# Kernel optimization log

Hardware: AMD Instinct MI355X
Metric: run time of the kernel (lower is better)

## Reference

```python
import jax, jax.numpy as jnp
import numpy as np

B, D, N, K, H = 32, 1024, 65536, 4096, 8

def setup_inputs() -> dict:
    key = jax.random.key(0)
    ks = jax.random.split(key, 8)
    s = D ** -0.5  # keep projections well-scaled
    return {
        "query": jax.random.normal(ks[0], (B, D), jnp.float32),
        "buffer": jax.random.normal(ks[1], (N, D), jnp.float32),
        "priorities": jax.random.normal(ks[2], (N,), jnp.float32),
        "Wq": jax.random.normal(ks[3], (D, D), jnp.float32) * s,
        "bq": jnp.zeros((D,), jnp.float32),
        "Wk": jax.random.normal(ks[4], (D, D), jnp.float32) * s,
        "bk": jnp.zeros((D,), jnp.float32),
        "Wv": jax.random.normal(ks[5], (D, D), jnp.float32) * s,
        "bv": jnp.zeros((D,), jnp.float32),
        "Wo": jax.random.normal(ks[6], (D, D), jnp.float32) * s,
        "bo": jnp.zeros((D,), jnp.float32),
        "top_k": K,
    }

def reference(query, buffer, priorities, Wq, bq, Wk, bk, Wv, bv, Wo, bo, top_k):
    # priority-based top-k selection (no_grad in original)
    _, idx = jax.lax.top_k(jax.lax.stop_gradient(priorities), top_k)
    subset = buffer[idx]                              # [K, D] gather; shared across batch
    hd = D // H
    scale = hd ** -0.5
    q = (query @ Wq + bq).reshape(B, H, hd)           # single-query attention (seq len 1)
    k = (subset @ Wk + bk).reshape(top_k, H, hd)
    v = (subset @ Wv + bv).reshape(top_k, H, hd)
    scores = jnp.einsum('bhd,khd->bhk', q, k) * scale  # [B, H, K]
    attn = jax.nn.softmax(scores, axis=-1)
    ctx = jnp.einsum('bhk,khd->bhd', attn, v).reshape(B, D)
    retrieved = ctx @ Wo + bo                          # [B, D]
    attn_avg = attn.mean(axis=1)                       # head-averaged weights [B, K]
    return retrieved, attn_avg
```

## Files before the change

kernel.cpp:

```cpp
#include <hip/hip_runtime.h>
#include <stdint.h>

typedef unsigned int u32;
typedef unsigned long long u64;
typedef uint16_t u16;

typedef short bf16x8 __attribute__((ext_vector_type(8)));
typedef float f32x4 __attribute__((ext_vector_type(4)));


__device__ __forceinline__ float bf2f(u16 x) { return __uint_as_float(((u32)x) << 16); }
__device__ __forceinline__ u16 f2bf(float f) {
    u32 u = __float_as_uint(f);
    return (u16)((u + 0x7FFF + ((u >> 16) & 1)) >> 16);
}


__global__ __launch_bounds__(256) void init_kernel(const float* __restrict__ prio,
                                                   u64* __restrict__ keys,
                                                   u32* __restrict__ hist,
                                                   u64* __restrict__ cand,
                                                   u32* __restrict__ scctl) {
    int i = blockIdx.x * 256 + threadIdx.x;
    u32 fb = __float_as_uint(prio[i]);
    u32 s = (fb & 0x80000000u) ? ~fb : (fb | 0x80000000u);
    keys[i] = ((u64)(~s) << 32) | (u64)i;
    hist[i] = 0;
    if (i < 8192) cand[i] = ~0ull;
    if (i < 4) scctl[i] = 0;
}

__global__ __launch_bounds__(256) void hist_kernel(const u64* __restrict__ keys,
                                                   u32* __restrict__ hist) {
    int i = blockIdx.x * 256 + threadIdx.x;
    atomicAdd(&hist[(u32)(keys[i] >> 48)], 1u);
}

__global__ __launch_bounds__(1024) void scan_kernel(const u32* __restrict__ hist,
                                                    u32* __restrict__ scctl) {
    int t = threadIdx.x;
    int base = t * 64;
    const uint4* hp = (const uint4*)(hist + base);
    u32 s = 0;
#pragma unroll
    for (int i = 0; i < 16; ++i) {
        uint4 h4 = hp[i];
        s += h4.x + h4.y + h4.z + h4.w;
    }
    u32 inc = s;
    for (int o = 1; o < 64; o <<= 1) {
        u32 v = __shfl_up(inc, o);
        if ((t & 63) >= o) inc += v;
    }
    __shared__ u32 ws[16];
    if ((t & 63) == 63) ws[t >> 6] = inc;
    __syncthreads();
    if (t == 0) {
        u32 a = 0;
        for (int wv = 0; wv < 16; ++wv) { u32 x = ws[wv]; ws[wv] = a; a += x; }
    }
    __syncthreads();
    u32 incl = inc + ws[t >> 6];
    u32 excl = incl - s;
    if (excl < 4096u && incl >= 4096u) {
        u32 cum = excl;
        for (int i = 0; i < 64; ++i) {
            u32 c = hist[base + i];
            if (cum + c >= 4096u) { scctl[0] = (u32)(base + i); scctl[1] = cum; break; }
            cum += c;
        }
    }
}

__global__ __launch_bounds__(256) void compact_kernel(const u64* __restrict__ keys,
                                                      u64* __restrict__ cand,
                                                      u32* __restrict__ scctl) {
    int i = blockIdx.x * 256 + threadIdx.x;
    u64 k = keys[i];
    u32 bin = (u32)(k >> 48);
    u32 Tb = scctl[0];
    if (bin < Tb) {
        u32 p = atomicAdd(&scctl[2], 1u);
        cand[p] = k;
    } else if (bin == Tb) {
        u32 p = atomicAdd(&scctl[3], 1u);
        if (p < 4096u) cand[4096 + p] = k;
    }
}

__global__ __launch_bounds__(1024) void sort4096_kernel(u64* __restrict__ cand) {
    __shared__ u64 sh[4096];
    u64* src = cand + (size_t)blockIdx.x * 4096;
    int t = threadIdx.x;
    u64 v[4];
#pragma unroll
    for (int s = 0; s < 4; ++s) v[s] = src[t * 4 + s];
    for (int k = 2; k <= 4096; k <<= 1) {
        for (int j = k >> 1; j >= 1; j >>= 1) {
            if (j >= 256) {
                __syncthreads();
#pragma unroll
                for (int s = 0; s < 4; ++s) sh[t * 4 + s] = v[s];
                __syncthreads();
#pragma unroll
                for (int s = 0; s < 4; ++s) {
                    int i = t * 4 + s;
                    u64 p = sh[i ^ j];
                    bool keepmin = (((i & k) == 0) == ((i & j) == 0));
                    v[s] = keepmin ? (v[s] < p ? v[s] : p) : (v[s] > p ? v[s] : p);
                }
            } else if (j >= 4) {
                int ld = j >> 2;
#pragma unroll
                for (int s = 0; s < 4; ++s) {
                    int i = t * 4 + s;
                    u64 p = __shfl_xor(v[s], ld, 64);
                    bool keepmin = (((i & k) == 0) == ((i & j) == 0));
                    v[s] = keepmin ? (v[s] < p ? v[s] : p) : (v[s] > p ? v[s] : p);
                }
            } else if (j == 2) {
#pragma unroll
                for (int s = 0; s < 2; ++s) {
                    int i = t * 4 + s;
                    bool up = ((i & k) == 0);
                    u64 a = v[s], b = v[s + 2];
                    if ((a > b) == up) { v[s] = b; v[s + 2] = a; }
                }
            } else {
#pragma unroll
                for (int s = 0; s < 4; s += 2) {
                    int i = t * 4 + s;
                    bool up = ((i & k) == 0);
                    u64 a = v[s], b = v[s + 1];
                    if ((a > b) == up) { v[s] = b; v[s + 1] = a; }
                }
            }
        }
    }
#pragma unroll
    for (int s = 0; s < 4; ++s) src[t * 4 + s] = v[s];
}

__global__ __launch_bounds__(256) void gather_transpose_kernel(const float* __restrict__ buffer,
                                                               const u64* __restrict__ cand,
                                                               const u32* __restrict__ scctl,
                                                               u16* __restrict__ bsub,
                                                               u16* __restrict__ bsubT) {
    int r0 = blockIdx.x * 32;
    int t = threadIdx.x;
    __shared__ u16 tile[32][65];
    __shared__ u32 rowidx[32];
    if (t < 32) {
        int row = r0 + t;
        u32 S = scctl[1];
        u64 key = ((u32)row < S) ? cand[row] : cand[4096 + row - (int)S];
        rowidx[t] = (u32)key;
    }
    __syncthreads();
    for (int c0 = 0; c0 < 1024; c0 += 64) {
        for (int s = t; s < 512; s += 256) {
            int r = s >> 4, c4 = (s & 15) * 4;
            float4 vv = *(const float4*)(buffer + (size_t)rowidx[r] * 1024 + c0 + c4);
            ushort4 o;
            o.x = f2bf(vv.x); o.y = f2bf(vv.y); o.z = f2bf(vv.z); o.w = f2bf(vv.w);
            *(ushort4*)(bsub + (size_t)(r0 + r) * 1024 + c0 + c4) = o;
            tile[r][c4] = o.x; tile[r][c4 + 1] = o.y; tile[r][c4 + 2] = o.z; tile[r][c4 + 3] = o.w;
        }
        __syncthreads();
        for (int s = t; s < 1024; s += 256) {
            int rT = s >> 4;
            int cT = (s & 15) * 2;
            ushort2 o2;
            o2.x = tile[cT][rT];
            o2.y = tile[cT + 1][rT];
            *(ushort2*)(bsubT + (size_t)(c0 + rT) * 4096 + r0 + cT) = o2;
        }
        __syncthreads();
    }
}

__global__ __launch_bounds__(256) void vecmat4_kernel(const float* __restrict__ X,
                                                      const float* __restrict__ W,
                                                      const float* __restrict__ bias,
                                                      float* __restrict__ out) {
    int bg = blockIdx.x, n0 = blockIdx.y * 64, t = threadIdx.x;
    __shared__ float xs[4][1024];
    __shared__ float red[4][4][64];
    for (int s = t; s < 4096; s += 256) {
        int bb = s >> 10, k = s & 1023;
        xs[bb][k] = X[(bg * 4 + bb) * 1024 + k];
    }
    __syncthreads();
    int n = t & 63, kq = t >> 6;
    const float* Wp = W + (size_t)(kq * 256) * 1024 + n0 + n;
    const float* x0 = xs[0] + kq * 256;
    const float* x1 = xs[1] + kq * 256;
    const float* x2 = xs[2] + kq * 256;
    const float* x3 = xs[3] + kq * 256;
    float a0 = 0.f, a1 = 0.f, a2 = 0.f, a3 = 0.f;
#pragma unroll 8
    for (int k = 0; k < 256; ++k) {
        float w = Wp[(size_t)k * 1024];
        a0 += x0[k] * w; a1 += x1[k] * w; a2 += x2[k] * w; a3 += x3[k] * w;
    }
    red[kq][0][n] = a0; red[kq][1][n] = a1; red[kq][2][n] = a2; red[kq][3][n] = a3;
    __syncthreads();
    int bb = t >> 6;
    out[(bg * 4 + bb) * 1024 + n0 + n] =
        red[0][bb][n] + red[1][bb][n] + red[2][bb][n] + red[3][bb][n] + bias[n0 + n];
}

__global__ __launch_bounds__(256) void s1_kernel(const float* __restrict__ qp,
                                                 const float* __restrict__ Wk,
                                                 const float* __restrict__ bk,
                                                 u16* __restrict__ S1,
                                                 float* __restrict__ cb) {
    int h = blockIdx.x, e0 = blockIdx.y * 64, t = threadIdx.x;
    __shared__ float qsh[32][128];
    __shared__ float wsh[64][132];
    for (int s = t; s < 4096; s += 256) {
        int b = s >> 7, d = s & 127;
        qsh[b][d] = qp[b * 1024 + h * 128 + d];
    }
    for (int s = t; s < 8192; s += 256) {
        int e = s >> 7, d = s & 127;
        wsh[e][d] = Wk[(size_t)(e0 + e) * 1024 + h * 128 + d];
    }
    __syncthreads();
    if (blockIdx.y == 0 && t < 32) {
        float a = 0.f;
        for (int d = 0; d < 128; ++d) a += qsh[t][d] * bk[h * 128 + d];
        cb[t * 8 + h] = a;
    }
    int e = t & 63, b0 = (t >> 6) * 8;
    float acc[8] = {0.f, 0.f, 0.f, 0.f, 0.f, 0.f, 0.f, 0.f};
#pragma unroll 4
    for (int d = 0; d < 128; d += 4) {
        float4 w = *(const float4*)&wsh[e][d];
#pragma unroll
        for (int bb = 0; bb < 8; ++bb) {
            float4 q = *(const float4*)&qsh[b0 + bb][d];
            acc[bb] += w.x * q.x + w.y * q.y + w.z * q.z + w.w * q.w;
        }
    }
#pragma unroll
    for (int bb = 0; bb < 8; ++bb)
        S1[(size_t)((b0 + bb) * 8 + h) * 1024 + e0 + e] = f2bf(acc[bb]);
}

__global__ __launch_bounds__(256) void gemm_scores_kernel(const u16* __restrict__ A,
                                                          const u16* __restrict__ B,
                                                          const float* __restrict__ cb,
                                                          float* __restrict__ out) {
    const int nt = blockIdx.x, mt = blockIdx.y;
    __shared__ __align__(16) u16 As[128 * 64];
    __shared__ __align__(16) u16 Bs[128 * 64];
    const int t = threadIdx.x, lane = t & 63, w = t >> 6;
    const int wm = (w >> 1) * 64, wn = (w & 1) * 64;
    const int q16 = lane >> 4, l15 = lane & 15;
    f32x4 acc[4][4];
#pragma unroll
    for (int i = 0; i < 4; i++)
#pragma unroll
        for (int j = 0; j < 4; j++) acc[i][j] = (f32x4){0.f, 0.f, 0.f, 0.f};
    const int sr = t >> 3, sc = t & 7;
    for (int kk = 0; kk < 1024; kk += 64) {
#pragma unroll
        for (int p = 0; p < 4; ++p) {
            int r = p * 32 + sr, pc = sc ^ (r & 7);
            uint4 va = *(const uint4*)(A + (size_t)(mt * 128 + r) * 1024 + kk + sc * 8);
            uint4 vb = *(const uint4*)(B + (size_t)(nt * 128 + r) * 1024 + kk + sc * 8);
            *(uint4*)&As[r * 64 + pc * 8] = va;
            *(uint4*)&Bs[r * 64 + pc * 8] = vb;
        }
        __syncthreads();
#pragma unroll
        for (int f = 0; f < 2; ++f) {
            bf16x8 a[4], b[4];
#pragma unroll
            for (int i = 0; i < 4; ++i) {
                int m = wm + i * 16 + l15;
                int pc = (f * 4 + q16) ^ (m & 7);
                a[i] = *(const bf16x8*)&As[m * 64 + pc * 8];
                int n = wn + i * 16 + l15;
                b[i] = *(const bf16x8*)&Bs[n * 64 + pc * 8];
            }
#pragma unroll
            for (int i = 0; i < 4; ++i)
#pragma unroll
                for (int j = 0; j < 4; ++j)
                    acc[i][j] = __builtin_amdgcn_mfma_f32_16x16x32_bf16(a[i], b[j], acc[i][j], 0, 0, 0);
        }
        __syncthreads();
    }
#pragma unroll
    for (int i = 0; i < 4; ++i) {
        int mbase = mt * 128 + wm + i * 16 + q16 * 4;
        float cbv[4];
#pragma unroll
        for (int r = 0; r < 4; ++r) cbv[r] = cb[mbase + r];
#pragma unroll
        for (int j = 0; j < 4; ++j) {
            int n = nt * 128 + wn + j * 16 + l15;
#pragma unroll
            for (int r = 0; r < 4; ++r)
                out[(size_t)(mbase + r) * 4096 + n] = acc[i][j][r] * 0.08838834764831845f + cbv[r];
        }
    }
}

__global__ __launch_bounds__(256) void softmax_kernel(const float* __restrict__ scores,
                                                      u16* __restrict__ attnbf) {
    int row = blockIdx.x, t = threadIdx.x;
    __shared__ float rowsh[4096];
    __shared__ float red[4];
    const float* p = scores + (size_t)row * 4096;
    float m = -1e30f;
    for (int i = t; i < 4096; i += 256) {
        float v = p[i];
        rowsh[i] = v;
        m = fmaxf(m, v);
    }
#pragma unroll
    for (int o = 32; o >= 1; o >>= 1) m = fmaxf(m, __shfl_xor(m, o));
    if ((t & 63) == 0) red[t >> 6] = m;
    __syncthreads();
    m = fmaxf(fmaxf(red[0], red[1]), fmaxf(red[2], red[3]));
    float sum = 0.f;
    for (int i = t; i < 4096; i += 256) {
        float e = __expf(rowsh[i] - m);
        rowsh[i] = e;
        sum += e;
    }
#pragma unroll
    for (int o = 32; o >= 1; o >>= 1) sum += __shfl_xor(sum, o);
    __syncthreads();
    if ((t & 63) == 0) red[t >> 6] = sum;
    __syncthreads();
    sum = red[0] + red[1] + red[2] + red[3];
    float inv = 1.0f / sum;
    for (int i = t; i < 4096; i += 256)
        attnbf[(size_t)row * 4096 + i] = f2bf(rowsh[i] * inv);
}

__global__ void attn_avg_kernel(const u16* __restrict__ attnbf,
                                float* __restrict__ out) {
    int g = blockIdx.x * 256 + threadIdx.x;
    int b = g >> 12, k = g & 4095;
    float s = 0.f;
#pragma unroll
    for (int h = 0; h < 8; ++h) s += bf2f(attnbf[(size_t)(b * 8 + h) * 4096 + k]);
    out[g] = s * 0.125f;
}

__global__ __launch_bounds__(256) void gemm_t_kernel(const u16* __restrict__ A,
                                                     const u16* __restrict__ B,
                                                     float* __restrict__ part) {
    const int nt = blockIdx.x, mt = blockIdx.y, ks = blockIdx.z;
    __shared__ __align__(16) u16 As[128 * 64];
    __shared__ __align__(16) u16 Bs[128 * 64];
    const int t = threadIdx.x, lane = t & 63, w = t >> 6;
    const int wm = (w >> 1) * 64, wn = (w & 1) * 64;
    const int q16 = lane >> 4, l15 = lane & 15;
    f32x4 acc[4][4];
#pragma unroll
    for (int i = 0; i < 4; i++)
#pragma unroll
        for (int j = 0; j < 4; j++) acc[i][j] = (f32x4){0.f, 0.f, 0.f, 0.f};
    const int sr = t >> 3, sc = t & 7;
    const int k0 = ks * 512;
    for (int kk = k0; kk < k0 + 512; kk += 64) {
#pragma unroll
        for (int p = 0; p < 4; ++p) {
            int r = p * 32 + sr, pc = sc ^ (r & 7);
            uint4 va = *(const uint4*)(A + (size_t)(mt * 128 + r) * 4096 + kk + sc * 8);
            uint4 vb = *(const uint4*)(B + (size_t)(nt * 128 + r) * 4096 + kk + sc * 8);
            *(uint4*)&As[r * 64 + pc * 8] = va;
            *(uint4*)&Bs[r * 64 + pc * 8] = vb;
        }
        __syncthreads();
#pragma unroll
        for (int f = 0; f < 2; ++f) {
            bf16x8 a[4], b[4];
#pragma unroll
            for (int i = 0; i < 4; ++i) {
                int m = wm + i * 16 + l15;
                int pc = (f * 4 + q16) ^ (m & 7);
                a[i] = *(const bf16x8*)&As[m * 64 + pc * 8];
                int n = wn + i * 16 + l15;
                b[i] = *(const bf16x8*)&Bs[n * 64 + pc * 8];
            }
#pragma unroll
            for (int i = 0; i < 4; ++i)
#pragma unroll
                for (int j = 0; j < 4; ++j)
                    acc[i][j] = __builtin_amdgcn_mfma_f32_16x16x32_bf16(a[i], b[j], acc[i][j], 0, 0, 0);
        }
        __syncthreads();
    }
#pragma unroll
    for (int i = 0; i < 4; ++i) {
        int mbase = mt * 128 + wm + i * 16 + q16 * 4;
#pragma unroll
        for (int j = 0; j < 4; ++j) {
            int n = nt * 128 + wn + j * 16 + l15;
#pragma unroll
            for (int r = 0; r < 4; ++r)
                part[(size_t)(ks * 256 + mbase + r) * 1024 + n] = acc[i][j][r];
        }
    }
}

__global__ __launch_bounds__(256) void ctx_reduce4_kernel(const float* __restrict__ part,
                                                          const float* __restrict__ Wv,
                                                          const float* __restrict__ bv,
                                                          float* __restrict__ ctx) {
    int bg = blockIdx.x, n0 = blockIdx.y * 64, t = threadIdx.x;
    int h = n0 >> 7;
    __shared__ float ts[4][1024];
    __shared__ float red[4][4][64];
    for (int s = t; s < 4096; s += 256) {
        int bb = s >> 10, e = s & 1023;
        int bh = (bg * 4 + bb) * 8 + h;
        float a = 0.f;
#pragma unroll
        for (int ks = 0; ks < 8; ++ks) a += part[(size_t)(ks * 256 + bh) * 1024 + e];
        ts[bb][e] = a;
    }
    __syncthreads();
    int n = t & 63, kq = t >> 6;
    const float* Wp = Wv + (size_t)(kq * 256) * 1024 + n0 + n;
    const float* x0 = ts[0] + kq * 256;
    const float* x1 = ts[1] + kq * 256;
    const float* x2 = ts[2] + kq * 256;
    const float* x3 = ts[3] + kq * 256;
    float a0 = 0.f, a1 = 0.f, a2 = 0.f, a3 = 0.f;
#pragma unroll 8
    for (int k = 0; k < 256; ++k) {
        float w = Wp[(size_t)k * 1024];
        a0 += x0[k] * w; a1 += x1[k] * w; a2 += x2[k] * w; a3 += x3[k] * w;
    }
    red[kq][0][n] = a0; red[kq][1][n] = a1; red[kq][2][n] = a2; red[kq][3][n] = a3;
    __syncthreads();
    int bb = t >> 6;
    ctx[(bg * 4 + bb) * 1024 + n0 + n] =
        red[0][bb][n] + red[1][bb][n] + red[2][bb][n] + red[3][bb][n] + bv[n0 + n];
}

extern "C" void kernel_launch(void* const* d_in, const int* in_sizes, int n_in,
                              void* d_out, int out_size, void* d_ws, size_t ws_size,
                              hipStream_t stream) {
    const float* query  = (const float*)d_in[0];
    const float* buffer = (const float*)d_in[1];
    const float* prio   = (const float*)d_in[2];
    const float* Wq     = (const float*)d_in[3];
    const float* bq     = (const float*)d_in[4];
    const float* Wk     = (const float*)d_in[5];
    const float* bk     = (const float*)d_in[6];
    const float* Wv     = (const float*)d_in[7];
    const float* bv     = (const float*)d_in[8];
    const float* Wo     = (const float*)d_in[9];
    const float* bo     = (const float*)d_in[10];

    char* w = (char*)d_ws;
    auto alloc = [&](size_t bytes) {
        char* p = w;
        w += (bytes + 255) & ~(size_t)255;
        return p;
    };
    u64* keys    = (u64*)alloc((size_t)65536 * 8);
    u32* hist    = (u32*)alloc((size_t)65536 * 4);
    u32* scctl   = (u32*)alloc(16);
    u64* cand    = (u64*)alloc((size_t)8192 * 8);
    u16* bsub    = (u16*)alloc((size_t)4096 * 1024 * 2);
    u16* bsubT   = (u16*)alloc((size_t)1024 * 4096 * 2);
    float* qp    = (float*)alloc((size_t)32 * 1024 * 4);
    u16* S1bf    = (u16*)alloc((size_t)256 * 1024 * 2);
    float* cbb   = (float*)alloc((size_t)256 * 4);
    float* scores= (float*)alloc((size_t)256 * 4096 * 4);
    u16* attnbf  = (u16*)alloc((size_t)256 * 4096 * 2);
    float* Tpart = (float*)alloc((size_t)8 * 256 * 1024 * 4);
    float* ctx   = (float*)alloc((size_t)32 * 1024 * 4);

    float* out_retrieved = (float*)d_out;
    float* out_attnavg   = (float*)d_out + 32768;

    init_kernel<<<256, 256, 0, stream>>>(prio, keys, hist, cand, scctl);
    hist_kernel<<<256, 256, 0, stream>>>(keys, hist);
    scan_kernel<<<1, 1024, 0, stream>>>(hist, scctl);
    compact_kernel<<<256, 256, 0, stream>>>(keys, cand, scctl);
    sort4096_kernel<<<2, 1024, 0, stream>>>(cand);

    gather_transpose_kernel<<<128, 256, 0, stream>>>(buffer, cand, scctl, bsub, bsubT);
    vecmat4_kernel<<<dim3(8, 16), 256, 0, stream>>>(query, Wq, bq, qp);

    s1_kernel<<<dim3(8, 16), 256, 0, stream>>>(qp, Wk, bk, S1bf, cbb);
    gemm_scores_kernel<<<dim3(32, 2), 256, 0, stream>>>(S1bf, bsub, cbb, scores);

    softmax_kernel<<<256, 256, 0, stream>>>(scores, attnbf);
    attn_avg_kernel<<<512, 256, 0, stream>>>(attnbf, out_attnavg);

    gemm_t_kernel<<<dim3(8, 2, 8), 256, 0, stream>>>(attnbf, bsubT, Tpart);
    ctx_reduce4_kernel<<<dim3(8, 16), 256, 0, stream>>>(Tpart, Wv, bv, ctx);

    vecmat4_kernel<<<dim3(8, 16), 256, 0, stream>>>(ctx, Wo, bo, out_retrieved);
}
```

Measured before the change: 557.3 us.

## Fuse independent kernels, drop key buffer, split-K scores GEMM, drop softmax-invariant bias

Merges independent stages into shared launches: init with the Q projection, the priority histogram with the S1 computation, and head-averaging with the attention-value GEMM. Priority keys are now recomputed from the priorities instead of stored in a 64-bit key array. The q·bk bias term is removed because softmax is shift-invariant within each row. The scores GEMM is split along K into two partials that the softmax sums, and the gather/transpose is rewritten to process 16 full rows per block with vectorized transposed stores. The aim is fewer launches, less traffic and more parallelism, at the cost of an extra partial-score buffer and a more heterogeneous mix of blocks within each kernel.

```diff
diff --git a/kernel.cpp b/kernel.cpp
--- a/kernel.cpp
+++ b/kernel.cpp
@@ -14,178 +14,18 @@
     u32 u = __float_as_uint(f);
     return (u16)((u + 0x7FFF + ((u >> 16) & 1)) >> 16);
 }
-
-
-__global__ __launch_bounds__(256) void init_kernel(const float* __restrict__ prio,
-                                                   u64* __restrict__ keys,
-                                                   u32* __restrict__ hist,
-                                                   u64* __restrict__ cand,
-                                                   u32* __restrict__ scctl) {
-    int i = blockIdx.x * 256 + threadIdx.x;
-    u32 fb = __float_as_uint(prio[i]);
+__device__ __forceinline__ u32 prio_key_hi(float pv) {
+    u32 fb = __float_as_uint(pv);
     u32 s = (fb & 0x80000000u) ? ~fb : (fb | 0x80000000u);
-    keys[i] = ((u64)(~s) << 32) | (u64)i;
-    hist[i] = 0;
-    if (i < 8192) cand[i] = ~0ull;
-    if (i < 4) scctl[i] = 0;
-}
-
-__global__ __launch_bounds__(256) void hist_kernel(const u64* __restrict__ keys,
-                                                   u32* __restrict__ hist) {
-    int i = blockIdx.x * 256 + threadIdx.x;
-    atomicAdd(&hist[(u32)(keys[i] >> 48)], 1u);
-}
-
-__global__ __launch_bounds__(1024) void scan_kernel(const u32* __restrict__ hist,
-                                                    u32* __restrict__ scctl) {
-    int t = threadIdx.x;
-    int base = t * 64;
-    const uint4* hp = (const uint4*)(hist + base);
-    u32 s = 0;
-#pragma unroll
-    for (int i = 0; i < 16; ++i) {
-        uint4 h4 = hp[i];
-        s += h4.x + h4.y + h4.z + h4.w;
-    }
-    u32 inc = s;
-    for (int o = 1; o < 64; o <<= 1) {
-        u32 v = __shfl_up(inc, o);
-        if ((t & 63) >= o) inc += v;
-    }
-    __shared__ u32 ws[16];
-    if ((t & 63) == 63) ws[t >> 6] = inc;
-    __syncthreads();
-    if (t == 0) {
-        u32 a = 0;
-        for (int wv = 0; wv < 16; ++wv) { u32 x = ws[wv]; ws[wv] = a; a += x; }
-    }
-    __syncthreads();
-    u32 incl = inc + ws[t >> 6];
-    u32 excl = incl - s;
-    if (excl < 4096u && incl >= 4096u) {
-        u32 cum = excl;
-        for (int i = 0; i < 64; ++i) {
-            u32 c = hist[base + i];
-            if (cum + c >= 4096u) { scctl[0] = (u32)(base + i); scctl[1] = cum; break; }
-            cum += c;
-        }
-    }
-}
-
-__global__ __launch_bounds__(256) void compact_kernel(const u64* __restrict__ keys,
-                                                      u64* __restrict__ cand,
-                                                      u32* __restrict__ scctl) {
-    int i = blockIdx.x * 256 + threadIdx.x;
-    u64 k = keys[i];
-    u32 bin = (u32)(k >> 48);
-    u32 Tb = scctl[0];
-    if (bin < Tb) {
-        u32 p = atomicAdd(&scctl[2], 1u);
-        cand[p] = k;
-    } else if (bin == Tb) {
-        u32 p = atomicAdd(&scctl[3], 1u);
-        if (p < 4096u) cand[4096 + p] = k;
-    }
-}
-
-__global__ __launch_bounds__(1024) void sort4096_kernel(u64* __restrict__ cand) {
-    __shared__ u64 sh[4096];
-    u64* src = cand + (size_t)blockIdx.x * 4096;
-    int t = threadIdx.x;
-    u64 v[4];
-#pragma unroll
-    for (int s = 0; s < 4; ++s) v[s] = src[t * 4 + s];
-    for (int k = 2; k <= 4096; k <<= 1) {
-        for (int j = k >> 1; j >= 1; j >>= 1) {
-            if (j >= 256) {
-                __syncthreads();
-#pragma unroll
-                for (int s = 0; s < 4; ++s) sh[t * 4 + s] = v[s];
-                __syncthreads();
-#pragma unroll
-                for (int s = 0; s < 4; ++s) {
-                    int i = t * 4 + s;
-                    u64 p = sh[i ^ j];
-                    bool keepmin = (((i & k) == 0) == ((i & j) == 0));
-                    v[s] = keepmin ? (v[s] < p ? v[s] : p) : (v[s] > p ? v[s] : p);
-                }
-            } else if (j >= 4) {
-                int ld = j >> 2;
-#pragma unroll
-                for (int s = 0; s < 4; ++s) {
-                    int i = t * 4 + s;
-                    u64 p = __shfl_xor(v[s], ld, 64);
-                    bool keepmin = (((i & k) == 0) == ((i & j) == 0));
-                    v[s] = keepmin ? (v[s] < p ? v[s] : p) : (v[s] > p ? v[s] : p);
-                }
-            } else if (j == 2) {
-#pragma unroll
-                for (int s = 0; s < 2; ++s) {
-                    int i = t * 4 + s;
-                    bool up = ((i & k) == 0);
-                    u64 a = v[s], b = v[s + 2];
-                    if ((a > b) == up) { v[s] = b; v[s + 2] = a; }
-                }
-            } else {
-#pragma unroll
-                for (int s = 0; s < 4; s += 2) {
-                    int i = t * 4 + s;
-                    bool up = ((i & k) == 0);
-                    u64 a = v[s], b = v[s + 1];
-                    if ((a > b) == up) { v[s] = b; v[s + 1] = a; }
-                }
-            }
-        }
-    }
-#pragma unroll
-    for (int s = 0; s < 4; ++s) src[t * 4 + s] = v[s];
-}
-
-__global__ __launch_bounds__(256) void gather_transpose_kernel(const float* __restrict__ buffer,
-                                                               const u64* __restrict__ cand,
-                                                               const u32* __restrict__ scctl,
-                                                               u16* __restrict__ bsub,
-                                                               u16* __restrict__ bsubT) {
-    int r0 = blockIdx.x * 32;
-    int t = threadIdx.x;
-    __shared__ u16 tile[32][65];
-    __shared__ u32 rowidx[32];
-    if (t < 32) {
-        int row = r0 + t;
-        u32 S = scctl[1];
-        u64 key = ((u32)row < S) ? cand[row] : cand[4096 + row - (int)S];
-        rowidx[t] = (u32)key;
-    }
-    __syncthreads();
-    for (int c0 = 0; c0 < 1024; c0 += 64) {
-        for (int s = t; s < 512; s += 256) {
-            int r = s >> 4, c4 = (s & 15) * 4;
-            float4 vv = *(const float4*)(buffer + (size_t)rowidx[r] * 1024 + c0 + c4);
-            ushort4 o;
-            o.x = f2bf(vv.x); o.y = f2bf(vv.y); o.z = f2bf(vv.z); o.w = f2bf(vv.w);
-            *(ushort4*)(bsub + (size_t)(r0 + r) * 1024 + c0 + c4) = o;
-            tile[r][c4] = o.x; tile[r][c4 + 1] = o.y; tile[r][c4 + 2] = o.z; tile[r][c4 + 3] = o.w;
-        }
-        __syncthreads();
-        for (int s = t; s < 1024; s += 256) {
-            int rT = s >> 4;
-            int cT = (s & 15) * 2;
-            ushort2 o2;
-            o2.x = tile[cT][rT];
-            o2.y = tile[cT + 1][rT];
-            *(ushort2*)(bsubT + (size_t)(c0 + rT) * 4096 + r0 + cT) = o2;
-        }
-        __syncthreads();
-    }
-}
-
-__global__ __launch_bounds__(256) void vecmat4_kernel(const float* __restrict__ X,
-                                                      const float* __restrict__ W,
-                                                      const float* __restrict__ bias,
-                                                      float* __restrict__ out) {
-    int bg = blockIdx.x, n0 = blockIdx.y * 64, t = threadIdx.x;
-    __shared__ float xs[4][1024];
-    __shared__ float red[4][4][64];
+    return ~s;
+}
+
+__device__ __forceinline__ void vecmat4_body(const float* __restrict__ X,
+                                             const float* __restrict__ W,
+                                             const float* __restrict__ bias,
+                                             float* __restrict__ out,
+                                             int bg, int n0, int t,
+                                             float (*xs)[1024], float (*red)[4][64]) {
     for (int s = t; s < 4096; s += 256) {
         int bb = s >> 10, k = s & 1023;
         xs[bb][k] = X[(bg * 4 + bb) * 1024 + k];
@@ -210,49 +50,217 @@
         red[0][bb][n] + red[1][bb][n] + red[2][bb][n] + red[3][bb][n] + bias[n0 + n];
 }
 
-__global__ __launch_bounds__(256) void s1_kernel(const float* __restrict__ qp,
-                                                 const float* __restrict__ Wk,
-                                                 const float* __restrict__ bk,
-                                                 u16* __restrict__ S1,
-                                                 float* __restrict__ cb) {
-    int h = blockIdx.x, e0 = blockIdx.y * 64, t = threadIdx.x;
+__global__ __launch_bounds__(256) void k1_init_qproj(const float* __restrict__ query,
+                                                     const float* __restrict__ Wq,
+                                                     const float* __restrict__ bq,
+                                                     float* __restrict__ qp,
+                                                     u32* __restrict__ hist,
+                                                     u64* __restrict__ cand,
+                                                     u32* __restrict__ scctl) {
+    __shared__ float xs[4][1024];
+    __shared__ float red[4][4][64];
+    int bid = blockIdx.x, t = threadIdx.x;
+    if (bid < 128) {
+        vecmat4_body(query, Wq, bq, qp, bid >> 4, (bid & 15) * 64, t, xs, red);
+    } else {
+        int id = bid - 128;
+        hist[id * 256 + t] = 0;
+        if (id < 32) cand[id * 256 + t] = ~0ull;
+        if (id == 32 && t < 8) scctl[t] = 0;
+    }
+}
+
+__global__ __launch_bounds__(256) void k2_hist_s1(const float* __restrict__ prio,
+                                                  const float* __restrict__ qp,
+                                                  const float* __restrict__ Wk,
+                                                  u16* __restrict__ S1,
+                                                  u32* __restrict__ hist) {
     __shared__ float qsh[32][128];
     __shared__ float wsh[64][132];
-    for (int s = t; s < 4096; s += 256) {
-        int b = s >> 7, d = s & 127;
-        qsh[b][d] = qp[b * 1024 + h * 128 + d];
-    }
-    for (int s = t; s < 8192; s += 256) {
-        int e = s >> 7, d = s & 127;
-        wsh[e][d] = Wk[(size_t)(e0 + e) * 1024 + h * 128 + d];
-    }
-    __syncthreads();
-    if (blockIdx.y == 0 && t < 32) {
-        float a = 0.f;
-        for (int d = 0; d < 128; ++d) a += qsh[t][d] * bk[h * 128 + d];
-        cb[t * 8 + h] = a;
-    }
-    int e = t & 63, b0 = (t >> 6) * 8;
-    float acc[8] = {0.f, 0.f, 0.f, 0.f, 0.f, 0.f, 0.f, 0.f};
+    int bid = blockIdx.x, t = threadIdx.x;
+    if (bid < 256) {
+        int i = bid * 256 + t;
+        u32 ds = prio_key_hi(prio[i]);
+        atomicAdd(&hist[ds >> 16], 1u);
+    } else {
+        int id = bid - 256;
+        int h = id & 7, e0 = (id >> 3) * 64;
+        for (int s = t; s < 4096; s += 256) {
+            int b = s >> 7, d = s & 127;
+            qsh[b][d] = qp[b * 1024 + h * 128 + d];
+        }
+        for (int s = t; s < 8192; s += 256) {
+            int e = s >> 7, d = s & 127;
+            wsh[e][d] = Wk[(size_t)(e0 + e) * 1024 + h * 128 + d];
+        }
+        __syncthreads();
+        int e = t & 63, b0 = (t >> 6) * 8;
+        float acc[8] = {0.f, 0.f, 0.f, 0.f, 0.f, 0.f, 0.f, 0.f};
 #pragma unroll 4
-    for (int d = 0; d < 128; d += 4) {
-        float4 w = *(const float4*)&wsh[e][d];
-#pragma unroll
-        for (int bb = 0; bb < 8; ++bb) {
-            float4 q = *(const float4*)&qsh[b0 + bb][d];
-            acc[bb] += w.x * q.x + w.y * q.y + w.z * q.z + w.w * q.w;
-        }
-    }
-#pragma unroll
-    for (int bb = 0; bb < 8; ++bb)
-        S1[(size_t)((b0 + bb) * 8 + h) * 1024 + e0 + e] = f2bf(acc[bb]);
-}
-
-__global__ __launch_bounds__(256) void gemm_scores_kernel(const u16* __restrict__ A,
-                                                          const u16* __restrict__ B,
-                                                          const float* __restrict__ cb,
-                                                          float* __restrict__ out) {
-    const int nt = blockIdx.x, mt = blockIdx.y;
+        for (int d = 0; d < 128; d += 4) {
+            float4 w = *(const float4*)&wsh[e][d];
+#pragma unroll
+            for (int bb = 0; bb < 8; ++bb) {
+                float4 q = *(const float4*)&qsh[b0 + bb][d];
+                acc[bb] += w.x * q.x + w.y * q.y + w.z * q.z + w.w * q.w;
+            }
+        }
+#pragma unroll
+        for (int bb = 0; bb < 8; ++bb)
+            S1[(size_t)((b0 + bb) * 8 + h) * 1024 + e0 + e] = f2bf(acc[bb]);
+    }
+}
+
+__global__ __launch_bounds__(1024) void scan_kernel(const u32* __restrict__ hist,
+                                                    u32* __restrict__ scctl) {
+    int t = threadIdx.x;
+    int base = t * 64;
+    const uint4* hp = (const uint4*)(hist + base);
+    u32 s = 0;
+#pragma unroll
+    for (int i = 0; i < 16; ++i) {
+        uint4 h4 = hp[i];
+        s += h4.x + h4.y + h4.z + h4.w;
+    }
+    u32 inc = s;
+    for (int o = 1; o < 64; o <<= 1) {
+        u32 v = __shfl_up(inc, o);
+        if ((t & 63) >= o) inc += v;
+    }
+    __shared__ u32 ws[16];
+    if ((t & 63) == 63) ws[t >> 6] = inc;
+    __syncthreads();
+    if (t == 0) {
+        u32 a = 0;
+        for (int wv = 0; wv < 16; ++wv) { u32 x = ws[wv]; ws[wv] = a; a += x; }
+    }
+    __syncthreads();
+    u32 incl = inc + ws[t >> 6];
+    u32 excl = incl - s;
+    if (excl < 4096u && incl >= 4096u) {
+        u32 cum = excl;
+        for (int i = 0; i < 64; ++i) {
+            u32 c = hist[base + i];
+            if (cum + c >= 4096u) { scctl[0] = (u32)(base + i); scctl[1] = cum; break; }
+            cum += c;
+        }
+    }
+}
+
+__global__ __launch_bounds__(256) void k4_compact(const float* __restrict__ prio,
+                                                  u64* __restrict__ cand,
+                                                  u32* __restrict__ scctl) {
+    int i = blockIdx.x * 256 + threadIdx.x;
+    u32 ds = prio_key_hi(prio[i]);
+    u64 k = ((u64)ds << 32) | (u64)i;
+    u32 bin = ds >> 16;
+    u32 Tb = scctl[0];
+    if (bin < Tb) {
+        cand[atomicAdd(&scctl[2], 1u)] = k;
+    } else if (bin == Tb) {
+        u32 p = atomicAdd(&scctl[3], 1u);
+        if (p < 4096u) cand[4096 + p] = k;
+    }
+}
+
+__global__ __launch_bounds__(1024) void sort4096_kernel(u64* __restrict__ cand) {
+    __shared__ u64 sh[4096];
+    u64* src = cand + (size_t)blockIdx.x * 4096;
+    int t = threadIdx.x;
+    u64 v[4];
+#pragma unroll
+    for (int s = 0; s < 4; ++s) v[s] = src[t * 4 + s];
+    for (int k = 2; k <= 4096; k <<= 1) {
+        for (int j = k >> 1; j >= 1; j >>= 1) {
+            if (j >= 256) {
+                __syncthreads();
+#pragma unroll
+                for (int s = 0; s < 4; ++s) sh[t * 4 + s] = v[s];
+                __syncthreads();
+#pragma unroll
+                for (int s = 0; s < 4; ++s) {
+                    int i = t * 4 + s;
+                    u64 p = sh[i ^ j];
+                    bool keepmin = (((i & k) == 0) == ((i & j) == 0));
+                    v[s] = keepmin ? (v[s] < p ? v[s] : p) : (v[s] > p ? v[s] : p);
+                }
+            } else if (j >= 4) {
+                int ld = j >> 2;
+#pragma unroll
+                for (int s = 0; s < 4; ++s) {
+                    int i = t * 4 + s;
+                    u64 p = __shfl_xor(v[s], ld, 64);
+                    bool keepmin = (((i & k) == 0) == ((i & j) == 0));
+                    v[s] = keepmin ? (v[s] < p ? v[s] : p) : (v[s] > p ? v[s] : p);
+                }
+            } else if (j == 2) {
+#pragma unroll
+                for (int s = 0; s < 2; ++s) {
+                    int i = t * 4 + s;
+                    bool up = ((i & k) == 0);
+                    u64 a = v[s], b = v[s + 2];
+                    if ((a > b) == up) { v[s] = b; v[s + 2] = a; }
+                }
+            } else {
+#pragma unroll
+                for (int s = 0; s < 4; s += 2) {
+                    int i = t * 4 + s;
+                    bool up = ((i & k) == 0);
+                    u64 a = v[s], b = v[s + 1];
+                    if ((a > b) == up) { v[s] = b; v[s + 1] = a; }
+                }
+            }
+        }
+    }
+#pragma unroll
+    for (int s = 0; s < 4; ++s) src[t * 4 + s] = v[s];
+}
+
+__global__ __launch_bounds__(256) void k6_gather(const float* __restrict__ buffer,
+                                                 const u64* __restrict__ cand,
+                                                 const u32* __restrict__ scctl,
+                                                 u16* __restrict__ bsub,
+                                                 u16* __restrict__ bsubT) {
+    int r0 = blockIdx.x * 16;
+    int t = threadIdx.x;
+    __shared__ __align__(16) u16 tile[16][1032];
+    __shared__ u32 rowidx[16];
+    if (t < 16) {
+        int row = r0 + t;
+        u32 S = scctl[1];
+        u64 key = ((u32)row < S) ? cand[row] : cand[4096 + row - (int)S];
+        rowidx[t] = (u32)key;
+    }
+    __syncthreads();
+    int r = t >> 4, cbase = (t & 15) * 4;
+    u32 ridx = rowidx[r];
+#pragma unroll
+    for (int it = 0; it < 16; ++it) {
+        int c4 = cbase + it * 64;
+        float4 vv = *(const float4*)(buffer + (size_t)ridx * 1024 + c4);
+        ushort4 o;
+        o.x = f2bf(vv.x); o.y = f2bf(vv.y); o.z = f2bf(vv.z); o.w = f2bf(vv.w);
+        *(ushort4*)(bsub + (size_t)(r0 + r) * 1024 + c4) = o;
+        *(ushort4*)&tile[r][c4] = o;
+    }
+    __syncthreads();
+#pragma unroll
+    for (int it = 0; it < 16; ++it) {
+        int wi = it * 256 + t;
+        int e = wi >> 2, kg = wi & 3;
+        ushort4 o;
+        o.x = tile[kg * 4 + 0][e];
+        o.y = tile[kg * 4 + 1][e];
+        o.z = tile[kg * 4 + 2][e];
+        o.w = tile[kg * 4 + 3][e];
+        *(ushort4*)(bsubT + (size_t)e * 4096 + r0 + kg * 4) = o;
+    }
+}
+
+__global__ __launch_bounds__(256) void k7_gemm_scores(const u16* __restrict__ A,
+                                                      const u16* __restrict__ B,
+                                                      float* __restrict__ spart) {
+    const int nt = blockIdx.x, mt = blockIdx.y, ks = blockIdx.z;
     __shared__ __align__(16) u16 As[128 * 64];
     __shared__ __align__(16) u16 Bs[128 * 64];
     const int t = threadIdx.x, lane = t & 63, w = t >> 6;
@@ -264,7 +272,8 @@
 #pragma unroll
         for (int j = 0; j < 4; j++) acc[i][j] = (f32x4){0.f, 0.f, 0.f, 0.f};
     const int sr = t >> 3, sc = t & 7;
-    for (int kk = 0; kk < 1024; kk += 64) {
+    const int k0 = ks * 512;
+    for (int kk = k0; kk < k0 + 512; kk += 64) {
 #pragma unroll
         for (int p = 0; p < 4; ++p) {
             int r = p * 32 + sr, pc = sc ^ (r & 7);
@@ -296,28 +305,26 @@
 #pragma unroll
     for (int i = 0; i < 4; ++i) {
         int mbase = mt * 128 + wm + i * 16 + q16 * 4;
-        float cbv[4];
-#pragma unroll
-        for (int r = 0; r < 4; ++r) cbv[r] = cb[mbase + r];
 #pragma unroll
         for (int j = 0; j < 4; ++j) {
             int n = nt * 128 + wn + j * 16 + l15;
 #pragma unroll
             for (int r = 0; r < 4; ++r)
-                out[(size_t)(mbase + r) * 4096 + n] = acc[i][j][r] * 0.08838834764831845f + cbv[r];
-        }
-    }
-}
-
-__global__ __launch_bounds__(256) void softmax_kernel(const float* __restrict__ scores,
-                                                      u16* __restrict__ attnbf) {
+                spart[(size_t)(ks * 256 + mbase + r) * 4096 + n] = acc[i][j][r];
+        }
+    }
+}
+
+__global__ __launch_bounds__(256) void k8_softmax(const float* __restrict__ spart,
+                                                  u16* __restrict__ attnbf) {
     int row = blockIdx.x, t = threadIdx.x;
     __shared__ float rowsh[4096];
     __shared__ float red[4];
-    const float* p = scores + (size_t)row * 4096;
+    const float* p0 = spart + (size_t)row * 4096;
+    const float* p1 = spart + (size_t)(256 + row) * 4096;
     float m = -1e30f;
     for (int i = t; i < 4096; i += 256) {
-        float v = p[i];
+        float v = (p0[i] + p1[i]) * 0.08838834764831845f;
         rowsh[i] = v;
         m = fmaxf(m, v);
     }
@@ -343,23 +350,24 @@
         attnbf[(size_t)row * 4096 + i] = f2bf(rowsh[i] * inv);
 }
 
-__global__ void attn_avg_kernel(const u16* __restrict__ attnbf,
-                                float* __restrict__ out) {
-    int g = blockIdx.x * 256 + threadIdx.x;
-    int b = g >> 12, k = g & 4095;
-    float s = 0.f;
-#pragma unroll
-    for (int h = 0; h < 8; ++h) s += bf2f(attnbf[(size_t)(b * 8 + h) * 4096 + k]);
-    out[g] = s * 0.125f;
-}
-
-__global__ __launch_bounds__(256) void gemm_t_kernel(const u16* __restrict__ A,
-                                                     const u16* __restrict__ B,
-                                                     float* __restrict__ part) {
-    const int nt = blockIdx.x, mt = blockIdx.y, ks = blockIdx.z;
+__global__ __launch_bounds__(256) void k9_gemmt_avg(const u16* __restrict__ A,
+                                                    const u16* __restrict__ B,
+                                                    float* __restrict__ part,
+                                                    float* __restrict__ avgout) {
     __shared__ __align__(16) u16 As[128 * 64];
     __shared__ __align__(16) u16 Bs[128 * 64];
-    const int t = threadIdx.x, lane = t & 63, w = t >> 6;
+    int bid = blockIdx.x, t = threadIdx.x;
+    if (bid >= 128) {
+        int g = (bid - 128) * 256 + t;
+        int b = g >> 12, k = g & 4095;
+        float s = 0.f;
+#pragma unroll
+        for (int h = 0; h < 8; ++h) s += bf2f(A[(size_t)(b * 8 + h) * 4096 + k]);
+        avgout[g] = s * 0.125f;
+        return;
+    }
+    const int nt = bid & 7, mt = (bid >> 3) & 1, ks = bid >> 4;
+    const int lane = t & 63, w = t >> 6;
     const int wm = (w >> 1) * 64, wn = (w & 1) * 64;
     const int q16 = lane >> 4, l15 = lane & 15;
     f32x4 acc[4][4];
@@ -447,6 +455,15 @@
         red[0][bb][n] + red[1][bb][n] + red[2][bb][n] + red[3][bb][n] + bv[n0 + n];
 }
 
+__global__ __launch_bounds__(256) void k11_outproj(const float* __restrict__ ctx,
+                                                   const float* __restrict__ Wo,
+                                                   const float* __restrict__ bo,
+                                                   float* __restrict__ out) {
+    __shared__ float xs[4][1024];
+    __shared__ float red[4][4][64];
+    vecmat4_body(ctx, Wo, bo, out, blockIdx.x, blockIdx.y * 64, threadIdx.x, xs, red);
+}
+
 extern "C" void kernel_launch(void* const* d_in, const int* in_sizes, int n_in,
                               void* d_out, int out_size, void* d_ws, size_t ws_size,
                               hipStream_t stream) {
@@ -456,7 +473,6 @@
     const float* Wq     = (const float*)d_in[3];
     const float* bq     = (const float*)d_in[4];
     const float* Wk     = (const float*)d_in[5];
-    const float* bk     = (const float*)d_in[6];
     const float* Wv     = (const float*)d_in[7];
     const float* bv     = (const float*)d_in[8];
     const float* Wo     = (const float*)d_in[9];
@@ -468,16 +484,14 @@
         w += (bytes + 255) & ~(size_t)255;
         return p;
     };
-    u64* keys    = (u64*)alloc((size_t)65536 * 8);
     u32* hist    = (u32*)alloc((size_t)65536 * 4);
-    u32* scctl   = (u32*)alloc(16);
+    u32* scctl   = (u32*)alloc(32);
     u64* cand    = (u64*)alloc((size_t)8192 * 8);
     u16* bsub    = (u16*)alloc((size_t)4096 * 1024 * 2);
     u16* bsubT   = (u16*)alloc((size_t)1024 * 4096 * 2);
     float* qp    = (float*)alloc((size_t)32 * 1024 * 4);
     u16* S1bf    = (u16*)alloc((size_t)256 * 1024 * 2);
-    float* cbb   = (float*)alloc((size_t)256 * 4);
-    float* scores= (float*)alloc((size_t)256 * 4096 * 4);
+    float* spart = (float*)alloc((size_t)2 * 256 * 4096 * 4);
     u16* attnbf  = (u16*)alloc((size_t)256 * 4096 * 2);
     float* Tpart = (float*)alloc((size_t)8 * 256 * 1024 * 4);
     float* ctx   = (float*)alloc((size_t)32 * 1024 * 4);
@@ -485,23 +499,15 @@
     float* out_retrieved = (float*)d_out;
     float* out_attnavg   = (float*)d_out + 32768;
 
-    init_kernel<<<256, 256, 0, stream>>>(prio, keys, hist, cand, scctl);
-    hist_kernel<<<256, 256, 0, stream>>>(keys, hist);
+    k1_init_qproj<<<384, 256, 0, stream>>>(query, Wq, bq, qp, hist, cand, scctl);
+    k2_hist_s1<<<384, 256, 0, stream>>>(prio, qp, Wk, S1bf, hist);
     scan_kernel<<<1, 1024, 0, stream>>>(hist, scctl);
-    compact_kernel<<<256, 256, 0, stream>>>(keys, cand, scctl);
+    k4_compact<<<256, 256, 0, stream>>>(prio, cand, scctl);
     sort4096_kernel<<<2, 1024, 0, stream>>>(cand);
-
-    gather_transpose_kernel<<<128, 256, 0, stream>>>(buffer, cand, scctl, bsub, bsubT);
-    vecmat4_kernel<<<dim3(8, 16), 256, 0, stream>>>(query, Wq, bq, qp);
-
-    s1_kernel<<<dim3(8, 16), 256, 0, stream>>>(qp, Wk, bk, S1bf, cbb);
-    gemm_scores_kernel<<<dim3(32, 2), 256, 0, stream>>>(S1bf, bsub, cbb, scores);
-
-    softmax_kernel<<<256, 256, 0, stream>>>(scores, attnbf);
-    attn_avg_kernel<<<512, 256, 0, stream>>>(attnbf, out_attnavg);
-
-    gemm_t_kernel<<<dim3(8, 2, 8), 256, 0, stream>>>(attnbf, bsubT, Tpart);
+    k6_gather<<<256, 256, 0, stream>>>(buffer, cand, scctl, bsub, bsubT);
+    k7_gemm_scores<<<dim3(32, 2, 2), 256, 0, stream>>>(S1bf, bsub, spart);
+    k8_softmax<<<256, 256, 0, stream>>>(spart, attnbf);
+    k9_gemmt_avg<<<640, 256, 0, stream>>>(attnbf, bsubT, Tpart, out_attnavg);
     ctx_reduce4_kernel<<<dim3(8, 16), 256, 0, stream>>>(Tpart, Wv, bv, ctx);
-
-    vecmat4_kernel<<<dim3(8, 16), 256, 0, stream>>>(ctx, Wo, bo, out_retrieved);
-}
+    k11_outproj<<<dim3(8, 16), 256, 0, stream>>>(ctx, Wo, bo, out_retrieved);
+}
```

Result: faster. 511.5 us (-8.2%).
